# Performance work log

Measured on AMD Instinct MI355X. Metric: run time of the kernel, lower is better.

The kernel has to match this reference:

```python
import jax, jax.numpy as jnp
import numpy as np

TAU = 2.0
EPS = 1e-5
SG_ALPHA = 4.0  # spikingjelly default Sigmoid surrogate alpha


@jax.custom_vjp
def heaviside(x):
    return (x >= 0.0).astype(x.dtype)

def _heaviside_fwd(x):
    return heaviside(x), x

def _heaviside_bwd(x, g):
    s = jax.nn.sigmoid(SG_ALPHA * x)
    return (g * SG_ALPHA * s * (1.0 - s),)

heaviside.defvjp(_heaviside_fwd, _heaviside_bwd)


def lif(x_seq, v_th):
    """Multi-step LIF, hard reset to 0, detach_reset=True. x_seq: (T, ...)."""
    def step(v, x_t):
        v = v + (x_t - v) / TAU
        s = heaviside(v - v_th)
        v = v * (1.0 - jax.lax.stop_gradient(s))  # detached hard reset
        return v, s
    _, spikes = jax.lax.scan(step, jnp.zeros_like(x_seq[0]), x_seq)
    return spikes


def bn(y, gamma, beta, mean, var):
    # y: (T, B, C, N); inference-mode BatchNorm1d over channel dim
    inv = gamma / jnp.sqrt(var + EPS)
    return y * inv[None, None, :, None] + (beta - mean * inv)[None, None, :, None]


def setup_inputs() -> dict:
    key = jax.random.key(0)
    ks = jax.random.split(key, 8)
    T, B, C, H, W = 4, 32, 256, 32, 32
    d = {
        "x": jax.random.normal(ks[0], (T, B, C, H, W), jnp.float32),
        "q_w": jax.random.normal(ks[1], (C, C), jnp.float32) * (1.0 / np.sqrt(C)),
        "q_gamma": jnp.ones((C,), jnp.float32),
        "q_beta": jnp.zeros((C,), jnp.float32),
        "q_mean": jnp.zeros((C,), jnp.float32),
        "q_var": jnp.ones((C,), jnp.float32),
        "k_w": jax.random.normal(ks[2], (C, C), jnp.float32) * (1.0 / np.sqrt(C)),
        "k_gamma": jnp.ones((C,), jnp.float32),
        "k_beta": jnp.zeros((C,), jnp.float32),
        "k_mean": jnp.zeros((C,), jnp.float32),
        "k_var": jnp.ones((C,), jnp.float32),
        "p_w": jax.random.normal(ks[3], (C, C), jnp.float32) * (1.0 / np.sqrt(C)),
        "p_b": jnp.zeros((C,), jnp.float32),
        "p_gamma": jnp.ones((C,), jnp.float32),
        "p_beta": jnp.zeros((C,), jnp.float32),
        "p_mean": jnp.zeros((C,), jnp.float32),
        "p_var": jnp.ones((C,), jnp.float32),
    }
    return d


def reference(x, q_w, q_gamma, q_beta, q_mean, q_var,
              k_w, k_gamma, k_beta, k_mean, k_var,
              p_w, p_b, p_gamma, p_beta, p_mean, p_var):
    T, B, C, H, W = x.shape
    num_heads = 8
    dh = C // num_heads
    N = H * W
    xs = x.reshape(T, B, C, N)

    # Q branch: 1x1 conv (C x C matmul) -> BN -> LIF
    q = bn(jnp.einsum('oc,tbcn->tbon', q_w, xs), q_gamma, q_beta, q_mean, q_var)
    q_spikes = lif(q, 1.0)                                # (T,B,C,N)
    q_h = q_spikes.reshape(T, B, num_heads, dh, N)

    # K branch
    k = bn(jnp.einsum('oc,tbcn->tbon', k_w, xs), k_gamma, k_beta, k_mean, k_var)
    k_spikes = lif(k, 1.0)
    k_h = k_spikes.reshape(T, B, num_heads, dh, N)

    # channel-sum pooled Q per head -> attn LIF (v_th=0.5) -> elementwise mult with K
    q_sum = jnp.sum(q_h, axis=3, keepdims=True)           # (T,B,h,1,N)
    attn = lif(q_sum, 0.5)
    x_one = attn * k_h                                    # (T,B,h,dh,N)

    # projection: 1x1 conv with bias -> BN -> LIF
    xo = x_one.reshape(T, B, C, N)
    xo = jnp.einsum('oc,tbcn->tbon', p_w, xo) + p_b[None, None, :, None]
    xo = bn(xo, p_gamma, p_beta, p_mean, p_var).reshape(T, B, C, H, W)
    x_final = lif(xo, 1.0)
    return x_final
```

## Files before the change

kernel.cpp:

```cpp
#include <hip/hip_runtime.h>
#include <cstdint>
#include <cstddef>

#define T_DIM 4
#define B_DIM 32
#define C_DIM 256
#define N_DIM 1024
#define NHEAD 8
#define DHEAD 32

__device__ __forceinline__ float lif_step(float& v, float x, float vth) {
    v = __fadd_rn(v, __fmul_rn(__fsub_rn(x, v), 0.5f));
    const float s = (v >= vth) ? 1.0f : 0.0f;
    if (s != 0.0f) v = 0.0f;
    return s;
}

__global__ __launch_bounds__(256) void k_qk(
    const float* __restrict__ x,
    const float* __restrict__ qw, const float* __restrict__ qg,
    const float* __restrict__ qbeta, const float* __restrict__ qmean, const float* __restrict__ qvar,
    const float* __restrict__ kw, const float* __restrict__ kg,
    const float* __restrict__ kbeta, const float* __restrict__ kmean, const float* __restrict__ kvar,
    uint8_t* __restrict__ xone)
{
    __shared__ float w_lds[64 * 64];
    __shared__ float x_lds[64 * 64];
    __shared__ float qsum_lds[64];
    __shared__ float attn_lds[64];

    const int tid = threadIdx.x;
    const int h   = blockIdx.x;
    const int nt  = blockIdx.y;
    const int b   = blockIdx.z;
    const int n0g = nt * 64;

    const int  mg   = tid >> 4;
    const int  m0   = mg << 2;
    const int  n0   = (tid & 15) << 2;
    const bool is_q = (mg < 8);

    float inv4[4], bias4[4];
    {
        const float* g  = is_q ? qg    : kg;
        const float* be = is_q ? qbeta : kbeta;
        const float* me = is_q ? qmean : kmean;
        const float* va = is_q ? qvar  : kvar;
        const int cb = h * DHEAD + (is_q ? m0 : (m0 - 32));
        #pragma unroll
        for (int i = 0; i < 4; i++) {
            const float iv = __fdiv_rn(g[cb + i], __fsqrt_rn(__fadd_rn(va[cb + i], 1e-5f)));
            inv4[i]  = iv;
            bias4[i] = __fsub_rn(be[cb + i], __fmul_rn(me[cb + i], iv));
        }
    }

    const int wo  = tid & 63;
    const int wkq = tid >> 6;
    const float* wrow = (wo < 32) ? (qw + (size_t)(h * DHEAD + wo) * C_DIM)
                                  : (kw + (size_t)(h * DHEAD + wo - 32) * C_DIM);
    const int xr  = tid >> 2;
    const int xcb = (tid & 3) << 4;

    float vstate[16];
    #pragma unroll
    for (int i = 0; i < 16; i++) vstate[i] = 0.0f;
    float v_attn = 0.0f;

    for (int t = 0; t < T_DIM; ++t) {
        float acc[16];
        #pragma unroll
        for (int i = 0; i < 16; i++) acc[i] = 0.0f;

        const float* xb = x + ((size_t)(t * B_DIM + b) * C_DIM) * N_DIM + n0g;

        for (int kk = 0; kk < C_DIM; kk += 64) {
            __syncthreads();
            if (kk == 0 && tid < 64) qsum_lds[tid] = 0.0f;
            #pragma unroll
            for (int j = 0; j < 4; j++) {
                const int k = (wkq << 4) + (j << 2);
                const float4 wv = *(const float4*)(wrow + kk + k);
                w_lds[(k + 0) * 64 + wo] = wv.x;
                w_lds[(k + 1) * 64 + wo] = wv.y;
                w_lds[(k + 2) * 64 + wo] = wv.z;
                w_lds[(k + 3) * 64 + wo] = wv.w;
            }
            #pragma unroll
            for (int j = 0; j < 4; j++) {
                *(float4*)(x_lds + xr * 64 + xcb + (j << 2)) =
                    *(const float4*)(xb + (size_t)(kk + xr) * N_DIM + xcb + (j << 2));
            }
            __syncthreads();
            #pragma unroll 4
            for (int k = 0; k < 64; k++) {
                const float4 a  = *(const float4*)(w_lds + k * 64 + m0);
                const float4 bv = *(const float4*)(x_lds + k * 64 + n0);
                acc[ 0] = fmaf(a.x, bv.x, acc[ 0]);
                acc[ 1] = fmaf(a.x, bv.y, acc[ 1]);
                acc[ 2] = fmaf(a.x, bv.z, acc[ 2]);
                acc[ 3] = fmaf(a.x, bv.w, acc[ 3]);
                acc[ 4] = fmaf(a.y, bv.x, acc[ 4]);
                acc[ 5] = fmaf(a.y, bv.y, acc[ 5]);
                acc[ 6] = fmaf(a.y, bv.z, acc[ 6]);
                acc[ 7] = fmaf(a.y, bv.w, acc[ 7]);
                acc[ 8] = fmaf(a.z, bv.x, acc[ 8]);
                acc[ 9] = fmaf(a.z, bv.y, acc[ 9]);
                acc[10] = fmaf(a.z, bv.z, acc[10]);
                acc[11] = fmaf(a.z, bv.w, acc[11]);
                acc[12] = fmaf(a.w, bv.x, acc[12]);
                acc[13] = fmaf(a.w, bv.y, acc[13]);
                acc[14] = fmaf(a.w, bv.z, acc[14]);
                acc[15] = fmaf(a.w, bv.w, acc[15]);
            }
        }

        float sarr[16];
        #pragma unroll
        for (int i = 0; i < 4; i++) {
            #pragma unroll
            for (int j = 0; j < 4; j++) {
                const float y = __fadd_rn(__fmul_rn(acc[i * 4 + j], inv4[i]), bias4[i]);
                sarr[i * 4 + j] = lif_step(vstate[i * 4 + j], y, 1.0f);
            }
        }

        if (is_q) {
            #pragma unroll
            for (int j = 0; j < 4; j++) {
                const float cs = sarr[j] + sarr[4 + j] + sarr[8 + j] + sarr[12 + j];
                atomicAdd(&qsum_lds[n0 + j], cs);
            }
        }
        __syncthreads();
        if (tid < 64) {
            attn_lds[tid] = lif_step(v_attn, qsum_lds[tid], 0.5f);
        }
        __syncthreads();
        if (!is_q) {
            #pragma unroll
            for (int i = 0; i < 4; i++) {
                uint32_t pack = 0;
                #pragma unroll
                for (int j = 0; j < 4; j++) {
                    if (sarr[i * 4 + j] != 0.0f && attn_lds[n0 + j] != 0.0f)
                        pack |= (1u << (8 * j));
                }
                const int c = h * DHEAD + (m0 - 32) + i;
                *(uint32_t*)(xone + ((size_t)(t * B_DIM + b) * C_DIM + c) * N_DIM + n0g + n0) = pack;
            }
        }
    }
}

__global__ __launch_bounds__(256) void k_proj(
    const uint8_t* __restrict__ xone,
    const float* __restrict__ pw, const float* __restrict__ pbias,
    const float* __restrict__ pg, const float* __restrict__ pbeta,
    const float* __restrict__ pmean, const float* __restrict__ pvar,
    float* __restrict__ out)
{
    __shared__ float w_lds[64 * 64];
    __shared__ float x_lds[64 * 64];

    const int tid = threadIdx.x;
    const int mt  = blockIdx.x;
    const int nt  = blockIdx.y;
    const int b   = blockIdx.z;
    const int n0g = nt * 64;
    const int c0  = mt * 64;

    const int mg = tid >> 4;
    const int m0 = mg << 2;
    const int n0 = (tid & 15) << 2;

    float inv4[4], bias4[4], pb4[4];
    #pragma unroll
    for (int i = 0; i < 4; i++) {
        const int c = c0 + m0 + i;
        const float iv = __fdiv_rn(pg[c], __fsqrt_rn(__fadd_rn(pvar[c], 1e-5f)));
        inv4[i]  = iv;
        bias4[i] = __fsub_rn(pbeta[c], __fmul_rn(pmean[c], iv));
        pb4[i]   = pbias[c];
    }

    const int wo  = tid & 63;
    const int wkq = tid >> 6;
    const float* wrow = pw + (size_t)(c0 + wo) * C_DIM;
    const int xr  = tid >> 2;
    const int xcb = (tid & 3) << 4;

    float vstate[16];
    #pragma unroll
    for (int i = 0; i < 16; i++) vstate[i] = 0.0f;

    for (int t = 0; t < T_DIM; ++t) {
        float acc[16];
        #pragma unroll
        for (int i = 0; i < 16; i++) acc[i] = 0.0f;

        const uint8_t* xb = xone + ((size_t)(t * B_DIM + b) * C_DIM) * N_DIM + n0g;

        for (int kk = 0; kk < C_DIM; kk += 64) {
            __syncthreads();
            #pragma unroll
            for (int j = 0; j < 4; j++) {
                const int k = (wkq << 4) + (j << 2);
                const float4 wv = *(const float4*)(wrow + kk + k);
                w_lds[(k + 0) * 64 + wo] = wv.x;
                w_lds[(k + 1) * 64 + wo] = wv.y;
                w_lds[(k + 2) * 64 + wo] = wv.z;
                w_lds[(k + 3) * 64 + wo] = wv.w;
            }
            {
                const uint4 pv = *(const uint4*)(xb + (size_t)(kk + xr) * N_DIM + xcb);
                const uint32_t u[4] = {pv.x, pv.y, pv.z, pv.w};
                #pragma unroll
                for (int j = 0; j < 4; j++) {
                    float4 f;
                    f.x = (float)( u[j]        & 0xffu);
                    f.y = (float)((u[j] >> 8 ) & 0xffu);
                    f.z = (float)((u[j] >> 16) & 0xffu);
                    f.w = (float)( u[j] >> 24        );
                    *(float4*)(x_lds + xr * 64 + xcb + (j << 2)) = f;
                }
            }
            __syncthreads();
            #pragma unroll 4
            for (int k = 0; k < 64; k++) {
                const float4 a  = *(const float4*)(w_lds + k * 64 + m0);
                const float4 bv = *(const float4*)(x_lds + k * 64 + n0);
                acc[ 0] = fmaf(a.x, bv.x, acc[ 0]);
                acc[ 1] = fmaf(a.x, bv.y, acc[ 1]);
                acc[ 2] = fmaf(a.x, bv.z, acc[ 2]);
                acc[ 3] = fmaf(a.x, bv.w, acc[ 3]);
                acc[ 4] = fmaf(a.y, bv.x, acc[ 4]);
                acc[ 5] = fmaf(a.y, bv.y, acc[ 5]);
                acc[ 6] = fmaf(a.y, bv.z, acc[ 6]);
                acc[ 7] = fmaf(a.y, bv.w, acc[ 7]);
                acc[ 8] = fmaf(a.z, bv.x, acc[ 8]);
                acc[ 9] = fmaf(a.z, bv.y, acc[ 9]);
                acc[10] = fmaf(a.z, bv.z, acc[10]);
                acc[11] = fmaf(a.z, bv.w, acc[11]);
                acc[12] = fmaf(a.w, bv.x, acc[12]);
                acc[13] = fmaf(a.w, bv.y, acc[13]);
                acc[14] = fmaf(a.w, bv.z, acc[14]);
                acc[15] = fmaf(a.w, bv.w, acc[15]);
            }
        }

        #pragma unroll
        for (int i = 0; i < 4; i++) {
            float s4[4];
            #pragma unroll
            for (int j = 0; j < 4; j++) {
                float y = __fadd_rn(acc[i * 4 + j], pb4[i]);
                y = __fadd_rn(__fmul_rn(y, inv4[i]), bias4[i]);
                s4[j] = lif_step(vstate[i * 4 + j], y, 1.0f);
            }
            const int c = c0 + m0 + i;
            float4 o4;
            o4.x = s4[0]; o4.y = s4[1]; o4.z = s4[2]; o4.w = s4[3];
            *(float4*)(out + ((size_t)(t * B_DIM + b) * C_DIM + c) * N_DIM + n0g + n0) = o4;
        }
    }
}

extern "C" void kernel_launch(void* const* d_in, const int* in_sizes, int n_in,
                              void* d_out, int out_size, void* d_ws, size_t ws_size,
                              hipStream_t stream) {
    const float* x     = (const float*)d_in[0];
    const float* q_w   = (const float*)d_in[1];
    const float* q_g   = (const float*)d_in[2];
    const float* q_b   = (const float*)d_in[3];
    const float* q_m   = (const float*)d_in[4];
    const float* q_v   = (const float*)d_in[5];
    const float* k_w   = (const float*)d_in[6];
    const float* k_g   = (const float*)d_in[7];
    const float* k_b   = (const float*)d_in[8];
    const float* k_m   = (const float*)d_in[9];
    const float* k_v   = (const float*)d_in[10];
    const float* p_w   = (const float*)d_in[11];
    const float* p_b   = (const float*)d_in[12];
    const float* p_g   = (const float*)d_in[13];
    const float* p_be  = (const float*)d_in[14];
    const float* p_m   = (const float*)d_in[15];
    const float* p_v   = (const float*)d_in[16];

    uint8_t* x_one = (uint8_t*)d_ws;
    float*   out   = (float*)d_out;

    dim3 g1(NHEAD, N_DIM / 64, B_DIM);
    k_qk<<<g1, 256, 0, stream>>>(x, q_w, q_g, q_b, q_m, q_v,
                                 k_w, k_g, k_b, k_m, k_v, x_one);

    dim3 g2(C_DIM / 64, N_DIM / 64, B_DIM);
    k_proj<<<g2, 256, 0, stream>>>(x_one, p_w, p_b, p_g, p_be, p_m, p_v, out);
}
```

Before: 962.2 us.

## Pre-transpose weights, use async global-to-LDS loads, bit-pack spike intermediate

Adds a small kernel that transposes the Q/K and projection weights once per call so both GEMM kernels can stage tiles with direct global-to-LDS async copies instead of register round-trips and scattered LDS stores. The Q/K kernel now packs the masked K spikes into 1-bit words through an LDS atomicOr and writes 32 words per row instead of a byte per element. The projection kernel unpacks those bits into floats. This cuts intermediate traffic by 8x and removes the transposing stores, at the cost of an extra launch, extra barriers and LDS atomics.

```diff
diff --git a/kernel.cpp b/kernel.cpp
--- a/kernel.cpp
+++ b/kernel.cpp
@@ -8,6 +8,7 @@
 #define N_DIM 1024
 #define NHEAD 8
 #define DHEAD 32
+#define NWRD 32
 
 __device__ __forceinline__ float lif_step(float& v, float x, float vth) {
     v = __fadd_rn(v, __fmul_rn(__fsub_rn(x, v), 0.5f));
@@ -16,23 +17,46 @@
     return s;
 }
 
+__device__ __forceinline__ void async_copy16(const float* g, float* l) {
+    __builtin_amdgcn_global_load_lds(
+        (const __attribute__((address_space(1))) unsigned int*)g,
+        (__attribute__((address_space(3))) unsigned int*)l, 16, 0, 0);
+}
+
+__global__ __launch_bounds__(256) void k_transpose(
+    const float* __restrict__ qw, const float* __restrict__ kw,
+    const float* __restrict__ pw, float* __restrict__ wqk_t,
+    float* __restrict__ p_t)
+{
+    const int i = blockIdx.x * 256 + threadIdx.x;
+    if (i < C_DIM * 512) {
+        const int k = i >> 9, col = i & 511;
+        const int h = col >> 6, j = col & 63;
+        wqk_t[i] = (j < 32) ? qw[(size_t)(h * 32 + j) * C_DIM + k]
+                            : kw[(size_t)(h * 32 + j - 32) * C_DIM + k];
+    } else {
+        const int i2 = i - C_DIM * 512;
+        const int k = i2 >> 8, c = i2 & 255;
+        p_t[i2] = pw[(size_t)c * C_DIM + k];
+    }
+}
+
 __global__ __launch_bounds__(256) void k_qk(
-    const float* __restrict__ x,
-    const float* __restrict__ qw, const float* __restrict__ qg,
-    const float* __restrict__ qbeta, const float* __restrict__ qmean, const float* __restrict__ qvar,
-    const float* __restrict__ kw, const float* __restrict__ kg,
-    const float* __restrict__ kbeta, const float* __restrict__ kmean, const float* __restrict__ kvar,
-    uint8_t* __restrict__ xone)
+    const float* __restrict__ x, const float* __restrict__ wqk,
+    const float* __restrict__ qg, const float* __restrict__ qbeta,
+    const float* __restrict__ qmean, const float* __restrict__ qvar,
+    const float* __restrict__ kg, const float* __restrict__ kbeta,
+    const float* __restrict__ kmean, const float* __restrict__ kvar,
+    uint32_t* __restrict__ xbits)
 {
     __shared__ float w_lds[64 * 64];
     __shared__ float x_lds[64 * 64];
     __shared__ float qsum_lds[64];
     __shared__ float attn_lds[64];
+    __shared__ uint32_t pack_lds[64];
 
     const int tid = threadIdx.x;
-    const int h   = blockIdx.x;
-    const int nt  = blockIdx.y;
-    const int b   = blockIdx.z;
+    const int h = blockIdx.x, nt = blockIdx.y, b = blockIdx.z;
     const int n0g = nt * 64;
 
     const int  mg   = tid >> 4;
@@ -55,12 +79,14 @@
         }
     }
 
-    const int wo  = tid & 63;
-    const int wkq = tid >> 6;
-    const float* wrow = (wo < 32) ? (qw + (size_t)(h * DHEAD + wo) * C_DIM)
-                                  : (kw + (size_t)(h * DHEAD + wo - 32) * C_DIM);
-    const int xr  = tid >> 2;
-    const int xcb = (tid & 3) << 4;
+    const int wid  = tid >> 6, lane = tid & 63;
+    const int lr   = lane >> 4;
+    const int lc   = (lane & 15) << 2;
+    const int rbase = wid * 16;
+
+    float* wl_dst = w_lds + rbase * 64;
+    float* xl_dst = x_lds + rbase * 64;
+    const float* wg0 = wqk + (size_t)(rbase + lr) * 512 + h * 64 + lc;
 
     float vstate[16];
     #pragma unroll
@@ -72,24 +98,13 @@
         #pragma unroll
         for (int i = 0; i < 16; i++) acc[i] = 0.0f;
 
-        const float* xb = x + ((size_t)(t * B_DIM + b) * C_DIM) * N_DIM + n0g;
+        const float* xg0 = x + ((size_t)(t * B_DIM + b) * C_DIM + rbase + lr) * N_DIM + n0g + lc;
 
         for (int kk = 0; kk < C_DIM; kk += 64) {
-            __syncthreads();
-            if (kk == 0 && tid < 64) qsum_lds[tid] = 0.0f;
-            #pragma unroll
-            for (int j = 0; j < 4; j++) {
-                const int k = (wkq << 4) + (j << 2);
-                const float4 wv = *(const float4*)(wrow + kk + k);
-                w_lds[(k + 0) * 64 + wo] = wv.x;
-                w_lds[(k + 1) * 64 + wo] = wv.y;
-                w_lds[(k + 2) * 64 + wo] = wv.z;
-                w_lds[(k + 3) * 64 + wo] = wv.w;
-            }
-            #pragma unroll
-            for (int j = 0; j < 4; j++) {
-                *(float4*)(x_lds + xr * 64 + xcb + (j << 2)) =
-                    *(const float4*)(xb + (size_t)(kk + xr) * N_DIM + xcb + (j << 2));
+            #pragma unroll
+            for (int i = 0; i < 4; i++) {
+                async_copy16(wg0 + (size_t)(kk + i * 4) * 512,   wl_dst + i * 256);
+                async_copy16(xg0 + (size_t)(kk + i * 4) * N_DIM, xl_dst + i * 256);
             }
             __syncthreads();
             #pragma unroll 4
@@ -113,6 +128,7 @@
                 acc[14] = fmaf(a.w, bv.z, acc[14]);
                 acc[15] = fmaf(a.w, bv.w, acc[15]);
             }
+            __syncthreads();
         }
 
         float sarr[16];
@@ -125,6 +141,9 @@
             }
         }
 
+        if (tid < 64) { qsum_lds[tid] = 0.0f; pack_lds[tid] = 0u; }
+        __syncthreads();
+
         if (is_q) {
             #pragma unroll
             for (int j = 0; j < 4; j++) {
@@ -133,45 +152,46 @@
             }
         }
         __syncthreads();
-        if (tid < 64) {
-            attn_lds[tid] = lif_step(v_attn, qsum_lds[tid], 0.5f);
-        }
+        if (tid < 64) attn_lds[tid] = lif_step(v_attn, qsum_lds[tid], 0.5f);
         __syncthreads();
+
         if (!is_q) {
             #pragma unroll
             for (int i = 0; i < 4; i++) {
-                uint32_t pack = 0;
+                uint32_t nib = 0;
                 #pragma unroll
                 for (int j = 0; j < 4; j++) {
                     if (sarr[i * 4 + j] != 0.0f && attn_lds[n0 + j] != 0.0f)
-                        pack |= (1u << (8 * j));
+                        nib |= (1u << j);
                 }
-                const int c = h * DHEAD + (m0 - 32) + i;
-                *(uint32_t*)(xone + ((size_t)(t * B_DIM + b) * C_DIM + c) * N_DIM + n0g + n0) = pack;
-            }
+                if (nib)
+                    atomicOr(&pack_lds[((m0 - 32) + i) * 2 + (n0 >> 5)], nib << (n0 & 31));
+            }
+        }
+        __syncthreads();
+        if (tid < 64) {
+            const int row = tid >> 1, word = tid & 1;
+            const int c = h * DHEAD + row;
+            xbits[((size_t)(t * B_DIM + b) * C_DIM + c) * NWRD + (n0g >> 5) + word] = pack_lds[tid];
         }
     }
 }
 
 __global__ __launch_bounds__(256) void k_proj(
-    const uint8_t* __restrict__ xone,
-    const float* __restrict__ pw, const float* __restrict__ pbias,
-    const float* __restrict__ pg, const float* __restrict__ pbeta,
-    const float* __restrict__ pmean, const float* __restrict__ pvar,
-    float* __restrict__ out)
+    const uint32_t* __restrict__ xbits, const float* __restrict__ pt,
+    const float* __restrict__ pbias, const float* __restrict__ pg,
+    const float* __restrict__ pbeta, const float* __restrict__ pmean,
+    const float* __restrict__ pvar, float* __restrict__ out)
 {
     __shared__ float w_lds[64 * 64];
     __shared__ float x_lds[64 * 64];
 
     const int tid = threadIdx.x;
-    const int mt  = blockIdx.x;
-    const int nt  = blockIdx.y;
-    const int b   = blockIdx.z;
+    const int mt = blockIdx.x, nt = blockIdx.y, b = blockIdx.z;
     const int n0g = nt * 64;
     const int c0  = mt * 64;
 
-    const int mg = tid >> 4;
-    const int m0 = mg << 2;
+    const int mg = tid >> 4, m0 = mg << 2;
     const int n0 = (tid & 15) << 2;
 
     float inv4[4], bias4[4], pb4[4];
@@ -184,11 +204,15 @@
         pb4[i]   = pbias[c];
     }
 
-    const int wo  = tid & 63;
-    const int wkq = tid >> 6;
-    const float* wrow = pw + (size_t)(c0 + wo) * C_DIM;
-    const int xr  = tid >> 2;
-    const int xcb = (tid & 3) << 4;
+    const int wid = tid >> 6, lane = tid & 63;
+    const int lr  = lane >> 4;
+    const int lc  = (lane & 15) << 2;
+    const int rbase = wid * 16;
+
+    float* wl_dst = w_lds + rbase * 64;
+    const float* wg0 = pt + (size_t)(rbase + lr) * 256 + c0 + lc;
+    const int wsel = (lane & 15) >> 3;
+    const int shf  = (lane & 7) * 4;
 
     float vstate[16];
     #pragma unroll
@@ -199,31 +223,22 @@
         #pragma unroll
         for (int i = 0; i < 16; i++) acc[i] = 0.0f;
 
-        const uint8_t* xb = xone + ((size_t)(t * B_DIM + b) * C_DIM) * N_DIM + n0g;
+        const uint32_t* xg0 = xbits + ((size_t)(t * B_DIM + b) * C_DIM + rbase + lr) * NWRD
+                              + (n0g >> 5) + wsel;
 
         for (int kk = 0; kk < C_DIM; kk += 64) {
-            __syncthreads();
-            #pragma unroll
-            for (int j = 0; j < 4; j++) {
-                const int k = (wkq << 4) + (j << 2);
-                const float4 wv = *(const float4*)(wrow + kk + k);
-                w_lds[(k + 0) * 64 + wo] = wv.x;
-                w_lds[(k + 1) * 64 + wo] = wv.y;
-                w_lds[(k + 2) * 64 + wo] = wv.z;
-                w_lds[(k + 3) * 64 + wo] = wv.w;
-            }
-            {
-                const uint4 pv = *(const uint4*)(xb + (size_t)(kk + xr) * N_DIM + xcb);
-                const uint32_t u[4] = {pv.x, pv.y, pv.z, pv.w};
-                #pragma unroll
-                for (int j = 0; j < 4; j++) {
-                    float4 f;
-                    f.x = (float)( u[j]        & 0xffu);
-                    f.y = (float)((u[j] >> 8 ) & 0xffu);
-                    f.z = (float)((u[j] >> 16) & 0xffu);
-                    f.w = (float)( u[j] >> 24        );
-                    *(float4*)(x_lds + xr * 64 + xcb + (j << 2)) = f;
-                }
+            #pragma unroll
+            for (int i = 0; i < 4; i++)
+                async_copy16(wg0 + (size_t)(kk + i * 4) * 256, wl_dst + i * 256);
+            #pragma unroll
+            for (int i = 0; i < 4; i++) {
+                const uint32_t wv = xg0[(size_t)(kk + i * 4) * NWRD];
+                float4 f;
+                f.x = ((wv >> (shf + 0)) & 1u) ? 1.0f : 0.0f;
+                f.y = ((wv >> (shf + 1)) & 1u) ? 1.0f : 0.0f;
+                f.z = ((wv >> (shf + 2)) & 1u) ? 1.0f : 0.0f;
+                f.w = ((wv >> (shf + 3)) & 1u) ? 1.0f : 0.0f;
+                *(float4*)(x_lds + (rbase + i * 4 + lr) * 64 + lc) = f;
             }
             __syncthreads();
             #pragma unroll 4
@@ -247,6 +262,7 @@
                 acc[14] = fmaf(a.w, bv.z, acc[14]);
                 acc[15] = fmaf(a.w, bv.w, acc[15]);
             }
+            __syncthreads();
         }
 
         #pragma unroll
@@ -269,31 +285,35 @@
 extern "C" void kernel_launch(void* const* d_in, const int* in_sizes, int n_in,
                               void* d_out, int out_size, void* d_ws, size_t ws_size,
                               hipStream_t stream) {
-    const float* x     = (const float*)d_in[0];
-    const float* q_w   = (const float*)d_in[1];
-    const float* q_g   = (const float*)d_in[2];
-    const float* q_b   = (const float*)d_in[3];
-    const float* q_m   = (const float*)d_in[4];
-    const float* q_v   = (const float*)d_in[5];
-    const float* k_w   = (const float*)d_in[6];
-    const float* k_g   = (const float*)d_in[7];
-    const float* k_b   = (const float*)d_in[8];
-    const float* k_m   = (const float*)d_in[9];
-    const float* k_v   = (const float*)d_in[10];
-    const float* p_w   = (const float*)d_in[11];
-    const float* p_b   = (const float*)d_in[12];
-    const float* p_g   = (const float*)d_in[13];
-    const float* p_be  = (const float*)d_in[14];
-    const float* p_m   = (const float*)d_in[15];
-    const float* p_v   = (const float*)d_in[16];
-
-    uint8_t* x_one = (uint8_t*)d_ws;
-    float*   out   = (float*)d_out;
+    const float* x    = (const float*)d_in[0];
+    const float* q_w  = (const float*)d_in[1];
+    const float* q_g  = (const float*)d_in[2];
+    const float* q_b  = (const float*)d_in[3];
+    const float* q_m  = (const float*)d_in[4];
+    const float* q_v  = (const float*)d_in[5];
+    const float* k_w  = (const float*)d_in[6];
+    const float* k_g  = (const float*)d_in[7];
+    const float* k_b  = (const float*)d_in[8];
+    const float* k_m  = (const float*)d_in[9];
+    const float* k_v  = (const float*)d_in[10];
+    const float* p_w  = (const float*)d_in[11];
+    const float* p_b  = (const float*)d_in[12];
+    const float* p_g  = (const float*)d_in[13];
+    const float* p_be = (const float*)d_in[14];
+    const float* p_m  = (const float*)d_in[15];
+    const float* p_v  = (const float*)d_in[16];
+
+    float*    wqk_t = (float*)d_ws;
+    float*    p_t   = (float*)((char*)d_ws + 524288);
+    uint32_t* xbits = (uint32_t*)((char*)d_ws + 786432);
+    float*    out   = (float*)d_out;
+
+    k_transpose<<<768, 256, 0, stream>>>(q_w, k_w, p_w, wqk_t, p_t);
 
     dim3 g1(NHEAD, N_DIM / 64, B_DIM);
-    k_qk<<<g1, 256, 0, stream>>>(x, q_w, q_g, q_b, q_m, q_v,
-                                 k_w, k_g, k_b, k_m, k_v, x_one);
+    k_qk<<<g1, 256, 0, stream>>>(x, wqk_t, q_g, q_b, q_m, q_v,
+                                 k_g, k_b, k_m, k_v, xbits);
 
     dim3 g2(C_DIM / 64, N_DIM / 64, B_DIM);
-    k_proj<<<g2, 256, 0, stream>>>(x_one, p_w, p_b, p_g, p_be, p_m, p_v, out);
-}
+    k_proj<<<g2, 256, 0, stream>>>(xbits, p_t, p_b, p_g, p_be, p_m, p_v, out);
+}
```

Measured after the change: 907.3 us. 5.7% less time.
